# Optimization experiments

Measured on AMD Instinct MI355X. Metric: run time of the kernel, lower is better.

The kernel has to match this reference:

```python
import jax, jax.numpy as jnp
import numpy as np

T, B, D_DEC, D_ENC = 2048, 128, 512, 512

def setup_inputs() -> dict:
    key = jax.random.key(0)
    k1, k2, k3, k4 = jax.random.split(key, 4)
    x = jax.random.normal(k1, (B, D_DEC), dtype=jnp.float32)
    encoder_states = jax.random.normal(k2, (T, B, D_ENC), dtype=jnp.float32)
    # nn.Linear(decoder_hidden_size, encoder_hidden_size): W [out,in], b [out]
    W = jax.random.normal(k3, (D_ENC, D_DEC), dtype=jnp.float32) / np.sqrt(D_DEC)
    b = jax.random.normal(k4, (D_ENC,), dtype=jnp.float32) * 0.01
    return {"x": x, "encoder_states": encoder_states, "W": W, "b": b}

def reference(x, encoder_states, W, b):
    # x: [B, D_dec] -> projected query xp: [B, E]
    xp = x @ W.T + b
    # scores[b,t] = sum_e xp[b,e] * enc[t,b,e]  (the Python loop, batched)
    scores = jnp.einsum('be,tbe->bt', xp, encoder_states)
    attn = jax.nn.softmax(scores, axis=1)                 # [B, T]
    context = jnp.einsum('bt,tbe->be', attn, encoder_states)  # [B, E]
    return jnp.concatenate([xp, context], axis=1)         # [B, 2E]
```

## Files before the change

kernel.cpp:

```cpp
#include <hip/hip_runtime.h>
#include <math.h>

#define T_DIM   2048
#define B_DIM   128
#define E_DIM   512
#define NSPLIT  16
#define TC      (T_DIM / NSPLIT)
#define TW      (TC / 4)
#define ROWS    4

typedef float floatx4 __attribute__((ext_vector_type(4)));

__device__ __forceinline__ float wave_reduce_sum(float v) {
    v += __shfl_xor(v, 1,  64);
    v += __shfl_xor(v, 2,  64);
    v += __shfl_xor(v, 4,  64);
    v += __shfl_xor(v, 8,  64);
    v += __shfl_xor(v, 16, 64);
    v += __shfl_xor(v, 32, 64);
    return v;
}

__device__ __forceinline__ float4 wave_reduce_sum4(float4 v) {
    #pragma unroll
    for (int mask = 1; mask < 64; mask <<= 1) {
        v.x += __shfl_xor(v.x, mask, 64);
        v.y += __shfl_xor(v.y, mask, 64);
        v.z += __shfl_xor(v.z, mask, 64);
        v.w += __shfl_xor(v.w, mask, 64);
    }
    return v;
}

__device__ __forceinline__ floatx4 nt_load4(const float* p) {
    return __builtin_nontemporal_load((const floatx4*)p);
}

__global__ __launch_bounds__(256) void proj_kernel(
    const float* __restrict__ x, const float* __restrict__ W,
    const float* __restrict__ bias, float* __restrict__ xp,
    float* __restrict__ out)
{
    const int b      = blockIdx.x;
    const int echunk = blockIdx.y;
    const int tid    = threadIdx.x;
    const int lane   = tid & 63;
    const int wave   = tid >> 6;

    const float4* x4 = (const float4*)(x + (size_t)b * E_DIM);
    const float4 xq0 = x4[lane];
    const float4 xq1 = x4[64 + lane];

    const int ebase = echunk * 128;
    for (int e = ebase + wave; e < ebase + 128; e += 4) {
        const float4* w4 = (const float4*)(W + (size_t)e * E_DIM);
        const float4 w0 = w4[lane];
        const float4 w1 = w4[64 + lane];
        float p = w0.x*xq0.x + w0.y*xq0.y + w0.z*xq0.z + w0.w*xq0.w;
        p      += w1.x*xq1.x + w1.y*xq1.y + w1.z*xq1.z + w1.w*xq1.w;
        p = wave_reduce_sum(p);
        if (lane == 0) {
            float v = p + bias[e];
            xp[(size_t)b * E_DIM + e] = v;
            out[(size_t)b * (2 * E_DIM) + e] = v;
        }
    }
}

__global__ __launch_bounds__(256) void attn_partial_kernel(
    const float* __restrict__ enc, const float* __restrict__ xp,
    float* __restrict__ m_part, float* __restrict__ l_part,
    float* __restrict__ acc_part)
{
    const int b    = blockIdx.x;
    const int s    = blockIdx.y;
    const int tid  = threadIdx.x;
    const int lane = tid & 63;
    const int wave = tid >> 6;

    const float4* xp4 = (const float4*)(xp + (size_t)b * E_DIM);
    const float4 xq0 = xp4[lane];
    const float4 xq1 = xp4[64 + lane];

    float m = -INFINITY;
    float l = 0.0f;
    float4 a0 = make_float4(0.f, 0.f, 0.f, 0.f);
    float4 a1 = make_float4(0.f, 0.f, 0.f, 0.f);

    const int t0 = s * TC + wave * TW;
    const size_t row_stride = (size_t)B_DIM * E_DIM;
    const float* base = enc + ((size_t)t0 * B_DIM + b) * E_DIM;

    #pragma unroll 1
    for (int i = 0; i < TW; i += ROWS) {
        floatx4 e0[ROWS], e1[ROWS];
        #pragma unroll
        for (int r = 0; r < ROWS; ++r) {
            const float* erow = base + (size_t)(i + r) * row_stride;
            e0[r] = nt_load4(erow + 4 * lane);
            e1[r] = nt_load4(erow + 4 * (64 + lane));
        }

        float4 d;
        {
            float t[ROWS];
            #pragma unroll
            for (int r = 0; r < ROWS; ++r) {
                t[r]  = e0[r].x*xq0.x + e0[r].y*xq0.y + e0[r].z*xq0.z + e0[r].w*xq0.w;
                t[r] += e1[r].x*xq1.x + e1[r].y*xq1.y + e1[r].z*xq1.z + e1[r].w*xq1.w;
            }
            d = make_float4(t[0], t[1], t[2], t[3]);
        }
        d = wave_reduce_sum4(d);

        const float mrow  = fmaxf(fmaxf(d.x, d.y), fmaxf(d.z, d.w));
        const float m_new = fmaxf(m, mrow);
        const float scale = __expf(m - m_new);
        const float p0 = __expf(d.x - m_new);
        const float p1 = __expf(d.y - m_new);
        const float p2 = __expf(d.z - m_new);
        const float p3 = __expf(d.w - m_new);
        l = l * scale + (p0 + p1 + p2 + p3);

        a0.x = a0.x*scale + p0*e0[0].x + p1*e0[1].x + p2*e0[2].x + p3*e0[3].x;
        a0.y = a0.y*scale + p0*e0[0].y + p1*e0[1].y + p2*e0[2].y + p3*e0[3].y;
        a0.z = a0.z*scale + p0*e0[0].z + p1*e0[1].z + p2*e0[2].z + p3*e0[3].z;
        a0.w = a0.w*scale + p0*e0[0].w + p1*e0[1].w + p2*e0[2].w + p3*e0[3].w;
        a1.x = a1.x*scale + p0*e1[0].x + p1*e1[1].x + p2*e1[2].x + p3*e1[3].x;
        a1.y = a1.y*scale + p0*e1[0].y + p1*e1[1].y + p2*e1[2].y + p3*e1[3].y;
        a1.z = a1.z*scale + p0*e1[0].z + p1*e1[1].z + p2*e1[2].z + p3*e1[3].z;
        a1.w = a1.w*scale + p0*e1[0].w + p1*e1[1].w + p2*e1[2].w + p3*e1[3].w;
        m = m_new;
    }

    __shared__ float lds_m[4];
    __shared__ float lds_l[4];
    __shared__ __align__(16) float lds_acc[4][E_DIM];

    if (lane == 0) lds_m[wave] = m;
    __syncthreads();
    const float M = fmaxf(fmaxf(lds_m[0], lds_m[1]), fmaxf(lds_m[2], lds_m[3]));
    const float wscale = __expf(m - M);

    float4* lacc = (float4*)&lds_acc[wave][0];
    lacc[lane]      = make_float4(a0.x*wscale, a0.y*wscale, a0.z*wscale, a0.w*wscale);
    lacc[64 + lane] = make_float4(a1.x*wscale, a1.y*wscale, a1.z*wscale, a1.w*wscale);
    if (lane == 0) lds_l[wave] = l * wscale;
    __syncthreads();

    const int pid = b * NSPLIT + s;
    if (tid == 0) {
        m_part[pid] = M;
        l_part[pid] = lds_l[0] + lds_l[1] + lds_l[2] + lds_l[3];
    }
    if (tid < 128) {
        float4 sum = make_float4(0.f, 0.f, 0.f, 0.f);
        for (int w = 0; w < 4; ++w) {
            const float4 v = ((const float4*)&lds_acc[w][0])[tid];
            sum.x += v.x; sum.y += v.y; sum.z += v.z; sum.w += v.w;
        }
        ((float4*)(acc_part + (size_t)pid * E_DIM))[tid] = sum;
    }
}

__global__ __launch_bounds__(128) void combine_kernel(
    const float* __restrict__ m_part, const float* __restrict__ l_part,
    const float* __restrict__ acc_part, float* __restrict__ out)
{
    const int b   = blockIdx.x;
    const int tid = threadIdx.x;

    float M = -INFINITY;
    for (int s = 0; s < NSPLIT; ++s) M = fmaxf(M, m_part[b * NSPLIT + s]);
    float w[NSPLIT];
    float L = 0.f;
    for (int s = 0; s < NSPLIT; ++s) {
        w[s] = __expf(m_part[b * NSPLIT + s] - M);
        L += w[s] * l_part[b * NSPLIT + s];
    }
    const float inv = 1.0f / L;

    float4 sum = make_float4(0.f, 0.f, 0.f, 0.f);
    for (int s = 0; s < NSPLIT; ++s) {
        const float4 v = ((const float4*)(acc_part + (size_t)(b * NSPLIT + s) * E_DIM))[tid];
        sum.x += w[s] * v.x; sum.y += w[s] * v.y;
        sum.z += w[s] * v.z; sum.w += w[s] * v.w;
    }
    const float4 r = make_float4(sum.x*inv, sum.y*inv, sum.z*inv, sum.w*inv);
    ((float4*)(out + (size_t)b * (2 * E_DIM) + E_DIM))[tid] = r;
}

extern "C" void kernel_launch(void* const* d_in, const int* in_sizes, int n_in,
                              void* d_out, int out_size, void* d_ws, size_t ws_size,
                              hipStream_t stream) {
    (void)in_sizes; (void)n_in; (void)out_size; (void)ws_size;
    const float* x    = (const float*)d_in[0];
    const float* enc  = (const float*)d_in[1];
    const float* W    = (const float*)d_in[2];
    const float* bias = (const float*)d_in[3];
    float* out = (float*)d_out;

    float* ws       = (float*)d_ws;
    float* xp       = ws;
    float* m_part   = ws + 65536;
    float* l_part   = ws + 65536 + 2048;
    float* acc_part = ws + 65536 + 4096;

    proj_kernel<<<dim3(B_DIM, 4), 256, 0, stream>>>(x, W, bias, xp, out);
    attn_partial_kernel<<<dim3(B_DIM, NSPLIT), 256, 0, stream>>>(enc, xp, m_part, l_part, acc_part);
    combine_kernel<<<B_DIM, 128, 0, stream>>>(m_part, l_part, acc_part, out);
}
```

Before: 693.7 us.

## Remap attention waves to batches and double-buffer encoder row loads

Each wave of the attention partial kernel now handles a different batch index (8 batches per 512-thread block) instead of four waves splitting the T range of one batch. This removes the in-block LDS cross-wave reduction, and NSPLIT doubles to 32 to keep the grid large. The main loop is software-pipelined with two register buffers so the next 4 rows load while the current 4 are computed. A __syncthreads per iteration keeps the waves in lockstep, which should make neighbouring batch rows hit memory together. The combine kernel merges its weight and accumulation loops and now reads twice as many partials.

```diff
diff --git a/kernel.cpp b/kernel.cpp
--- a/kernel.cpp
+++ b/kernel.cpp
@@ -4,9 +4,9 @@
 #define T_DIM   2048
 #define B_DIM   128
 #define E_DIM   512
-#define NSPLIT  16
+#define NSPLIT  32
 #define TC      (T_DIM / NSPLIT)
-#define TW      (TC / 4)
+#define GB      8
 #define ROWS    4
 
 typedef float floatx4 __attribute__((ext_vector_type(4)));
@@ -67,16 +67,63 @@
     }
 }
 
-__global__ __launch_bounds__(256) void attn_partial_kernel(
+__device__ __forceinline__ void load_rows(
+    const float* __restrict__ base, size_t row_stride, int i, int lane,
+    floatx4 (&e0)[ROWS], floatx4 (&e1)[ROWS])
+{
+    #pragma unroll
+    for (int r = 0; r < ROWS; ++r) {
+        const float* erow = base + (size_t)(i + r) * row_stride;
+        e0[r] = nt_load4(erow + 4 * lane);
+        e1[r] = nt_load4(erow + 4 * (64 + lane));
+    }
+}
+
+__device__ __forceinline__ void compute_rows(
+    const floatx4 (&e0)[ROWS], const floatx4 (&e1)[ROWS],
+    const float4 xq0, const float4 xq1,
+    float& m, float& l, float4& a0, float4& a1)
+{
+    float t[ROWS];
+    #pragma unroll
+    for (int r = 0; r < ROWS; ++r) {
+        t[r]  = e0[r].x*xq0.x + e0[r].y*xq0.y + e0[r].z*xq0.z + e0[r].w*xq0.w;
+        t[r] += e1[r].x*xq1.x + e1[r].y*xq1.y + e1[r].z*xq1.z + e1[r].w*xq1.w;
+    }
+    float4 d = make_float4(t[0], t[1], t[2], t[3]);
+    d = wave_reduce_sum4(d);
+
+    const float mrow  = fmaxf(fmaxf(d.x, d.y), fmaxf(d.z, d.w));
+    const float m_new = fmaxf(m, mrow);
+    const float scale = __expf(m - m_new);
+    const float p0 = __expf(d.x - m_new);
+    const float p1 = __expf(d.y - m_new);
+    const float p2 = __expf(d.z - m_new);
+    const float p3 = __expf(d.w - m_new);
+    l = l * scale + (p0 + p1 + p2 + p3);
+
+    a0.x = a0.x*scale + p0*e0[0].x + p1*e0[1].x + p2*e0[2].x + p3*e0[3].x;
+    a0.y = a0.y*scale + p0*e0[0].y + p1*e0[1].y + p2*e0[2].y + p3*e0[3].y;
+    a0.z = a0.z*scale + p0*e0[0].z + p1*e0[1].z + p2*e0[2].z + p3*e0[3].z;
+    a0.w = a0.w*scale + p0*e0[0].w + p1*e0[1].w + p2*e0[2].w + p3*e0[3].w;
+    a1.x = a1.x*scale + p0*e1[0].x + p1*e1[1].x + p2*e1[2].x + p3*e1[3].x;
+    a1.y = a1.y*scale + p0*e1[0].y + p1*e1[1].y + p2*e1[2].y + p3*e1[3].y;
+    a1.z = a1.z*scale + p0*e1[0].z + p1*e1[1].z + p2*e1[2].z + p3*e1[3].z;
+    a1.w = a1.w*scale + p0*e1[0].w + p1*e1[1].w + p2*e1[2].w + p3*e1[3].w;
+    m = m_new;
+}
+
+__global__ __launch_bounds__(512, 4) void attn_partial_kernel(
     const float* __restrict__ enc, const float* __restrict__ xp,
     float* __restrict__ m_part, float* __restrict__ l_part,
     float* __restrict__ acc_part)
 {
-    const int b    = blockIdx.x;
+    const int bg   = blockIdx.x;
     const int s    = blockIdx.y;
     const int tid  = threadIdx.x;
     const int lane = tid & 63;
     const int wave = tid >> 6;
+    const int b    = bg * GB + wave;
 
     const float4* xp4 = (const float4*)(xp + (size_t)b * E_DIM);
     const float4 xq0 = xp4[lane];
@@ -87,80 +134,32 @@
     float4 a0 = make_float4(0.f, 0.f, 0.f, 0.f);
     float4 a1 = make_float4(0.f, 0.f, 0.f, 0.f);
 
-    const int t0 = s * TC + wave * TW;
     const size_t row_stride = (size_t)B_DIM * E_DIM;
-    const float* base = enc + ((size_t)t0 * B_DIM + b) * E_DIM;
+    const float* base = enc + ((size_t)(s * TC) * B_DIM + b) * E_DIM;
+
+    floatx4 ea0[ROWS], ea1[ROWS];
+    floatx4 eb0[ROWS], eb1[ROWS];
+
+    load_rows(base, row_stride, 0, lane, ea0, ea1);
 
     #pragma unroll 1
-    for (int i = 0; i < TW; i += ROWS) {
-        floatx4 e0[ROWS], e1[ROWS];
-        #pragma unroll
-        for (int r = 0; r < ROWS; ++r) {
-            const float* erow = base + (size_t)(i + r) * row_stride;
-            e0[r] = nt_load4(erow + 4 * lane);
-            e1[r] = nt_load4(erow + 4 * (64 + lane));
-        }
-
-        float4 d;
-        {
-            float t[ROWS];
-            #pragma unroll
-            for (int r = 0; r < ROWS; ++r) {
-                t[r]  = e0[r].x*xq0.x + e0[r].y*xq0.y + e0[r].z*xq0.z + e0[r].w*xq0.w;
-                t[r] += e1[r].x*xq1.x + e1[r].y*xq1.y + e1[r].z*xq1.z + e1[r].w*xq1.w;
-            }
-            d = make_float4(t[0], t[1], t[2], t[3]);
-        }
-        d = wave_reduce_sum4(d);
-
-        const float mrow  = fmaxf(fmaxf(d.x, d.y), fmaxf(d.z, d.w));
-        const float m_new = fmaxf(m, mrow);
-        const float scale = __expf(m - m_new);
-        const float p0 = __expf(d.x - m_new);
-        const float p1 = __expf(d.y - m_new);
-        const float p2 = __expf(d.z - m_new);
-        const float p3 = __expf(d.w - m_new);
-        l = l * scale + (p0 + p1 + p2 + p3);
-
-        a0.x = a0.x*scale + p0*e0[0].x + p1*e0[1].x + p2*e0[2].x + p3*e0[3].x;
-        a0.y = a0.y*scale + p0*e0[0].y + p1*e0[1].y + p2*e0[2].y + p3*e0[3].y;
-        a0.z = a0.z*scale + p0*e0[0].z + p1*e0[1].z + p2*e0[2].z + p3*e0[3].z;
-        a0.w = a0.w*scale + p0*e0[0].w + p1*e0[1].w + p2*e0[2].w + p3*e0[3].w;
-        a1.x = a1.x*scale + p0*e1[0].x + p1*e1[1].x + p2*e1[2].x + p3*e1[3].x;
-        a1.y = a1.y*scale + p0*e1[0].y + p1*e1[1].y + p2*e1[2].y + p3*e1[3].y;
-        a1.z = a1.z*scale + p0*e1[0].z + p1*e1[1].z + p2*e1[2].z + p3*e1[3].z;
-        a1.w = a1.w*scale + p0*e1[0].w + p1*e1[1].w + p2*e1[2].w + p3*e1[3].w;
-        m = m_new;
-    }
-
-    __shared__ float lds_m[4];
-    __shared__ float lds_l[4];
-    __shared__ __align__(16) float lds_acc[4][E_DIM];
-
-    if (lane == 0) lds_m[wave] = m;
-    __syncthreads();
-    const float M = fmaxf(fmaxf(lds_m[0], lds_m[1]), fmaxf(lds_m[2], lds_m[3]));
-    const float wscale = __expf(m - M);
-
-    float4* lacc = (float4*)&lds_acc[wave][0];
-    lacc[lane]      = make_float4(a0.x*wscale, a0.y*wscale, a0.z*wscale, a0.w*wscale);
-    lacc[64 + lane] = make_float4(a1.x*wscale, a1.y*wscale, a1.z*wscale, a1.w*wscale);
-    if (lane == 0) lds_l[wave] = l * wscale;
-    __syncthreads();
+    for (int i = 0; i < TC; i += 2 * ROWS) {
+        load_rows(base, row_stride, i + ROWS, lane, eb0, eb1);
+        compute_rows(ea0, ea1, xq0, xq1, m, l, a0, a1);
+        if (i + 2 * ROWS < TC)
+            load_rows(base, row_stride, i + 2 * ROWS, lane, ea0, ea1);
+        compute_rows(eb0, eb1, xq0, xq1, m, l, a0, a1);
+        __syncthreads();
+    }
 
     const int pid = b * NSPLIT + s;
-    if (tid == 0) {
-        m_part[pid] = M;
-        l_part[pid] = lds_l[0] + lds_l[1] + lds_l[2] + lds_l[3];
-    }
-    if (tid < 128) {
-        float4 sum = make_float4(0.f, 0.f, 0.f, 0.f);
-        for (int w = 0; w < 4; ++w) {
-            const float4 v = ((const float4*)&lds_acc[w][0])[tid];
-            sum.x += v.x; sum.y += v.y; sum.z += v.z; sum.w += v.w;
-        }
-        ((float4*)(acc_part + (size_t)pid * E_DIM))[tid] = sum;
-    }
+    if (lane == 0) {
+        m_part[pid] = m;
+        l_part[pid] = l;
+    }
+    float4* dst = (float4*)(acc_part + (size_t)pid * E_DIM);
+    dst[lane]      = a0;
+    dst[64 + lane] = a1;
 }
 
 __global__ __launch_bounds__(128) void combine_kernel(
@@ -172,20 +171,17 @@
 
     float M = -INFINITY;
     for (int s = 0; s < NSPLIT; ++s) M = fmaxf(M, m_part[b * NSPLIT + s]);
-    float w[NSPLIT];
+
     float L = 0.f;
-    for (int s = 0; s < NSPLIT; ++s) {
-        w[s] = __expf(m_part[b * NSPLIT + s] - M);
-        L += w[s] * l_part[b * NSPLIT + s];
-    }
-    const float inv = 1.0f / L;
-
     float4 sum = make_float4(0.f, 0.f, 0.f, 0.f);
     for (int s = 0; s < NSPLIT; ++s) {
+        const float wi = __expf(m_part[b * NSPLIT + s] - M);
+        L += wi * l_part[b * NSPLIT + s];
         const float4 v = ((const float4*)(acc_part + (size_t)(b * NSPLIT + s) * E_DIM))[tid];
-        sum.x += w[s] * v.x; sum.y += w[s] * v.y;
-        sum.z += w[s] * v.z; sum.w += w[s] * v.w;
-    }
+        sum.x += wi * v.x; sum.y += wi * v.y;
+        sum.z += wi * v.z; sum.w += wi * v.w;
+    }
+    const float inv = 1.0f / L;
     const float4 r = make_float4(sum.x*inv, sum.y*inv, sum.z*inv, sum.w*inv);
     ((float4*)(out + (size_t)b * (2 * E_DIM) + E_DIM))[tid] = r;
 }
@@ -203,10 +199,10 @@
     float* ws       = (float*)d_ws;
     float* xp       = ws;
     float* m_part   = ws + 65536;
-    float* l_part   = ws + 65536 + 2048;
-    float* acc_part = ws + 65536 + 4096;
+    float* l_part   = ws + 65536 + 4096;
+    float* acc_part = ws + 65536 + 8192;
 
     proj_kernel<<<dim3(B_DIM, 4), 256, 0, stream>>>(x, W, bias, xp, out);
-    attn_partial_kernel<<<dim3(B_DIM, NSPLIT), 256, 0, stream>>>(enc, xp, m_part, l_part, acc_part);
+    attn_partial_kernel<<<dim3(B_DIM / GB, NSPLIT), 512, 0, stream>>>(enc, xp, m_part, l_part, acc_part);
     combine_kernel<<<B_DIM, 128, 0, stream>>>(m_part, l_part, acc_part, out);
 }
```

Measured after the change: 716.4 us. 1.03x slower.
